# Kernel optimization log

Measured on AMD Instinct MI355X. Metric: run time of the kernel, lower is better.

Reference implementation:

```python
import jax, jax.numpy as jnp
import numpy as np

B, N = 32, 512
IN, HID, HEADS, OUT = 128, 32, 4, 128
NEG_SLOPE = 0.2


def _ln(x, g, b, eps=1e-5):
    mu = x.mean(-1, keepdims=True)
    var = ((x - mu) ** 2).mean(-1, keepdims=True)
    return (x - mu) * jax.lax.rsqrt(var + eps) * g + b


def _gat(x, adj_mask, W, a_src, a_dst, average):
    # x: [B,N,F], adj_mask: [B,1,N,N] bool, W: [F,H,D], a_*: [H,D]
    h = jnp.einsum('bnf,fhd->bnhd', x, W)                      # [B,N,H,D]
    e_src = jnp.einsum('bnhd,hd->bhn', h, a_src)               # [B,H,N]
    e_dst = jnp.einsum('bnhd,hd->bhn', h, a_dst)
    e = jax.nn.leaky_relu(e_src[:, :, :, None] + e_dst[:, :, None, :], NEG_SLOPE)  # [B,H,N,N]
    e = jnp.where(adj_mask, e, jnp.asarray(-1e9, e.dtype))
    att = jax.nn.softmax(e, axis=-1)                           # masked softmax over neighbors
    out = jnp.einsum('bhnm,bmhd->bnhd', att, h)                # aggregate neighbor features
    if average:
        return out.mean(axis=2)                                # [B,N,D]
    return out.reshape(out.shape[0], out.shape[1], -1)         # concat heads [B,N,H*D]


def setup_inputs() -> dict:
    key = jax.random.key(0)
    ks = jax.random.split(key, 16)
    def nrm(k, shape, scale=0.05):
        return jax.random.normal(k, shape, dtype=jnp.float32) * scale
    return {
        'x': jax.random.normal(ks[0], (B, N, IN), dtype=jnp.float32),
        'graph': jax.random.randint(ks[1], (B, N, N), 0, 2, dtype=jnp.int32),
        'W0': nrm(ks[2], (IN, HEADS, HID)),
        'a_src0': nrm(ks[3], (HEADS, HID)),
        'a_dst0': nrm(ks[4], (HEADS, HID)),
        'W1': nrm(ks[5], (HEADS * HID, 1, OUT)),
        'a_src1': nrm(ks[6], (1, OUT)),
        'a_dst1': nrm(ks[7], (1, OUT)),
        'ln1_g': jnp.ones((IN + OUT,), jnp.float32), 'ln1_b': jnp.zeros((IN + OUT,), jnp.float32),
        'lin_W': nrm(ks[8], (IN + OUT, OUT)), 'lin_b': jnp.zeros((OUT,), jnp.float32),
        'me_W0': nrm(ks[9], (OUT, OUT)), 'me_b0': jnp.zeros((OUT,), jnp.float32),
        'me_W1': nrm(ks[10], (OUT, OUT)), 'me_b1': jnp.zeros((OUT,), jnp.float32),
        'ln2_g': jnp.ones((OUT,), jnp.float32), 'ln2_b': jnp.zeros((OUT,), jnp.float32),
        'oh_W': nrm(ks[11], (OUT, OUT)), 'oh_b': jnp.zeros((OUT,), jnp.float32),
        'ln3_g': jnp.ones((OUT,), jnp.float32), 'ln3_b': jnp.zeros((OUT,), jnp.float32),
    }


def reference(x, graph, W0, a_src0, a_dst0, W1, a_src1, a_dst1,
              ln1_g, ln1_b, lin_W, lin_b, me_W0, me_b0, me_W1, me_b1,
              ln2_g, ln2_b, oh_W, oh_b, ln3_g, ln3_b):
    eye = jnp.eye(N, dtype=bool)
    adj_mask = ((graph > 0) | eye)[:, None, :, :]              # self-loops, [B,1,N,N]
    m = _gat(x, adj_mask, W0, a_src0, a_dst0, average=False)   # [B,N,HEADS*HID]
    m = jax.nn.elu(m)
    m = _gat(m, adj_mask, W1, a_src1, a_dst1, average=True)    # [B,N,OUT]
    m = _ln(jnp.concatenate([x, m], axis=-1), ln1_g, ln1_b)    # ln1
    m = m @ lin_W + lin_b                                      # linear
    enc = jax.nn.gelu(m @ me_W0 + me_b0, approximate=False) @ me_W1 + me_b1
    out = _ln(m + enc, ln2_g, ln2_b)                           # ln2(residual)
    out = jax.nn.gelu(out @ oh_W + oh_b, approximate=False)
    out = _ln(out, ln3_g, ln3_b)                               # LN inside output_head
    return out
```

## Files before the change

kernel.cpp:

```cpp
#include <hip/hip_runtime.h>
#include <cmath>


typedef unsigned short ushort_t;
typedef __attribute__((ext_vector_type(8))) short short8;
typedef __attribute__((ext_vector_type(4))) float f32x4;

__device__ __forceinline__ float gelu_f(float v) {
    return 0.5f * v * (1.0f + erff(v * 0.70710678118654752f));
}
__device__ __forceinline__ ushort_t f2bf(float x) {
    union { float f; unsigned u; } v; v.f = x;
    return (ushort_t)((v.u + 0x7FFFu + ((v.u >> 16) & 1u)) >> 16);
}
__device__ __forceinline__ ushort_t f2bf_t(float x) {
    union { float f; unsigned u; } v; v.f = x;
    return (ushort_t)(v.u >> 16);
}

__global__ __launch_bounds__(256) void prep_wt(const float* __restrict__ lin_W,
        const float* __restrict__ me_W0, const float* __restrict__ me_W1,
        const float* __restrict__ oh_W, const float* __restrict__ W0,
        const float* __restrict__ W1, ushort_t* __restrict__ WT) {
    int i = blockIdx.x * 256 + threadIdx.x;
    if (i < 32768)       { int c = i >> 8, k = i & 255;                   WT[i] = f2bf(lin_W[k * 128 + c]); }
    else if (i < 49152)  { int j = i - 32768;  int c = j >> 7, k = j & 127; WT[i] = f2bf(me_W0[k * 128 + c]); }
    else if (i < 65536)  { int j = i - 49152;  int c = j >> 7, k = j & 127; WT[i] = f2bf(me_W1[k * 128 + c]); }
    else if (i < 81920)  { int j = i - 65536;  int c = j >> 7, k = j & 127; WT[i] = f2bf(oh_W[k * 128 + c]); }
    else if (i < 98304)  { int j = i - 81920;  int c = j >> 7, k = j & 127; WT[i] = f2bf(W0[k * 128 + c]); }
    else if (i < 114688) { int j = i - 98304;  int c = j >> 7, k = j & 127; WT[i] = f2bf(W1[k * 128 + c]); }
}

__global__ __launch_bounds__(256) void pack_graph(const int* __restrict__ g,
                                                  unsigned* __restrict__ gm) {
    int idx = blockIdx.x * 256 + threadIdx.x;
    const int4* gp = (const int4*)g + (size_t)idx * 8;
    unsigned m = 0;
#pragma unroll
    for (int q = 0; q < 8; q++) {
        int4 v = gp[q];
        m |= (unsigned)(v.x > 0) << (q * 4 + 0);
        m |= (unsigned)(v.y > 0) << (q * 4 + 1);
        m |= (unsigned)(v.z > 0) << (q * 4 + 2);
        m |= (unsigned)(v.w > 0) << (q * 4 + 3);
    }
    gm[idx] = m;
}

__global__ __launch_bounds__(256) void gemm_mfma0(const float* __restrict__ X,
        const ushort_t* __restrict__ WTr, ushort_t* __restrict__ Ht,
        const float* __restrict__ a_s, const float* __restrict__ a_d,
        float* __restrict__ es, float* __restrict__ ed) {
    __shared__ __align__(16) ushort_t abuf[16 * 128];
    __shared__ __align__(16) ushort_t tb[128 * 24];
    __shared__ float2 ered[8 * 16];
    const int tid = threadIdx.x;
    const int row0 = blockIdx.x * 16;
    const int b = row0 >> 9, m0 = row0 & 511;
    const int w = tid >> 6, lane = tid & 63;
    const int quad = lane >> 4, lid = lane & 15;
    {
        int r = tid >> 4, g = tid & 15;
        const float4* src = (const float4*)(X + (row0 + r) * 128 + g * 8);
        float4 a = src[0], bb = src[1];
        short8 p;
        p[0] = (short)f2bf(a.x);  p[1] = (short)f2bf(a.y);
        p[2] = (short)f2bf(a.z);  p[3] = (short)f2bf(a.w);
        p[4] = (short)f2bf(bb.x); p[5] = (short)f2bf(bb.y);
        p[6] = (short)f2bf(bb.z); p[7] = (short)f2bf(bb.w);
        *(short8*)&abuf[r * 128 + ((g ^ (r & 7)) * 8)] = p;
    }
    __syncthreads();
    short8 af[4];
#pragma unroll
    for (int kc = 0; kc < 4; kc++)
        af[kc] = *(const short8*)&abuf[lid * 128 + (((kc * 4 + quad) ^ (lid & 7)) * 8)];
    f32x4 C[2];
#pragma unroll
    for (int i = 0; i < 2; i++) {
        int ct = w + 4 * i;
        const ushort_t* bp = WTr + (ct * 16 + lid) * 128 + quad * 8;
        C[i] = (f32x4){0.f, 0.f, 0.f, 0.f};
#pragma unroll
        for (int kc = 0; kc < 4; kc++) {
            short8 bf = *(const short8*)&bp[kc * 32];
            C[i] = __builtin_amdgcn_mfma_f32_16x16x32_bf16(af[kc], bf, C[i], 0, 0, 0);
        }
    }
#pragma unroll
    for (int i = 0; i < 2; i++) {
        int ct = w + 4 * i, col = ct * 16 + lid;
        float as_c = a_s[col], ad_c = a_d[col];
        float s0[4], d0[4];
#pragma unroll
        for (int r = 0; r < 4; r++) { s0[r] = C[i][r] * as_c; d0[r] = C[i][r] * ad_c; }
#pragma unroll
        for (int st = 1; st <= 8; st <<= 1)
#pragma unroll
            for (int r = 0; r < 4; r++) {
                s0[r] += __shfl_xor(s0[r], st);
                d0[r] += __shfl_xor(d0[r], st);
            }
        if (lid == 0) {
#pragma unroll
            for (int r = 0; r < 4; r++)
                ered[ct * 16 + quad * 4 + r] = make_float2(s0[r], d0[r]);
        }
#pragma unroll
        for (int r = 0; r < 4; r++)
            tb[col * 24 + quad * 4 + r] = f2bf(C[i][r]);
    }
    __syncthreads();
    if (tid < 64) {
        int row = tid & 15, h = tid >> 4;
        float2 pa = ered[(2 * h) * 16 + row], pb = ered[(2 * h + 1) * 16 + row];
        es[(b * 4 + h) * 512 + m0 + row] = pa.x + pb.x;
        ed[(b * 4 + h) * 512 + m0 + row] = pa.y + pb.y;
    }
    {
        int c = tid >> 1, half = tid & 1;
        *(short8*)&Ht[b * 65536 + c * 512 + m0 + half * 8] = *(const short8*)&tb[c * 24 + half * 8];
    }
}

__global__ __launch_bounds__(256) void gat0_gemm(const ushort_t* __restrict__ Ht0,
        const float* __restrict__ es0, const float* __restrict__ ed0,
        const unsigned* __restrict__ gmask, const ushort_t* __restrict__ W1T,
        const float* __restrict__ a_s, const float* __restrict__ a_d,
        ushort_t* __restrict__ Ht1, float* __restrict__ es1, float* __restrict__ ed1) {
    __shared__ __align__(16) char smem[33024];
    ushort_t* hsb  = (ushort_t*)smem;
    ushort_t* ps   = (ushort_t*)(smem + 16384);
    float*    eds  = (float*)(smem + 24576);
    float*    ess  = (float*)(smem + 32768);
    ushort_t* abuf = (ushort_t*)(smem + 16384);
    ushort_t* tb   = (ushort_t*)(smem + 24576);
    float2*   ered = (float2*)(smem + 30720);
    const int tid = threadIdx.x;
    const int b = blockIdx.y, n0 = blockIdx.x * 16;
    const int wv = tid >> 6, lane = tid & 63;
    const int quad = lane >> 4, lid = lane & 15;
    const int pn = tid >> 4, pg = (tid >> 1) & 7, ph = tid & 1;
    for (int i = tid; i < 2048; i += 256) eds[i] = ed0[b * 2048 + i];
    if (tid < 64) ess[tid] = es0[b * 2048 + (tid >> 4) * 512 + n0 + (tid & 15)];
    const unsigned* gmrow = gmask + (b * 512 + n0 + pn) * 16;
    const short8 onesf = {0x3F80, 0x3F80, 0x3F80, 0x3F80, 0x3F80, 0x3F80, 0x3F80, 0x3F80};
    f32x4 acc[2], dsf;
    acc[0] = (f32x4){0.f, 0.f, 0.f, 0.f};
    acc[1] = (f32x4){0.f, 0.f, 0.f, 0.f};
    dsf = (f32x4){0.f, 0.f, 0.f, 0.f};
    for (int mc = 0; mc < 512; mc += 64) {
        __syncthreads();
        {
            const ushort_t* src = Ht0 + b * 65536 + mc;
            for (int u = tid; u < 1024; u += 256) {
                int c = u >> 3, g = u & 7;
                *(short8*)&hsb[c * 64 + ((g ^ (c & 7)) * 8)] = *(const short8*)&src[c * 512 + g * 8];
            }
        }
        {
            int ng = n0 + pn, mbase = mc + pg * 8;
            unsigned mw = gmrow[mbase >> 5];
            unsigned mbits = (mw >> (mbase & 31)) & 0xffu;
            if ((unsigned)(ng - mbase) < 8u) mbits |= 1u << (ng - mbase);
#pragma unroll
            for (int hi = 0; hi < 2; hi++) {
                int hh = ph * 2 + hi;
                float es_v = ess[hh * 16 + pn];
                float4 e0v = *(const float4*)&eds[hh * 512 + mbase];
                float4 e1v = *(const float4*)&eds[hh * 512 + mbase + 4];
                float ev[8] = {e0v.x, e0v.y, e0v.z, e0v.w, e1v.x, e1v.y, e1v.z, e1v.w};
                short8 pk;
#pragma unroll
                for (int j = 0; j < 8; j++) {
                    float e = es_v + ev[j];
                    e = fmaxf(e, 0.2f * e);
                    e = ((mbits >> j) & 1u) ? e : -1e30f;
                    pk[j] = (short)f2bf_t(__expf(e));
                }
                int prow = hh * 16 + pn;
                *(short8*)&ps[prow * 64 + ((pg ^ (prow & 7)) * 8)] = pk;
            }
        }
        __syncthreads();
#pragma unroll
        for (int kc = 0; kc < 2; kc++) {
            const int gsw = ((kc * 4 + quad) ^ (lid & 7)) * 8;
            short8 a = *(const short8*)&ps[(wv * 16 + lid) * 64 + gsw];
            short8 b0 = *(const short8*)&hsb[(wv * 32 + lid) * 64 + gsw];
            short8 b1 = *(const short8*)&hsb[(wv * 32 + 16 + lid) * 64 + gsw];
            acc[0] = __builtin_amdgcn_mfma_f32_16x16x32_bf16(a, b0, acc[0], 0, 0, 0);
            acc[1] = __builtin_amdgcn_mfma_f32_16x16x32_bf16(a, b1, acc[1], 0, 0, 0);
            dsf = __builtin_amdgcn_mfma_f32_16x16x32_bf16(a, onesf, dsf, 0, 0, 0);
        }
    }
    __syncthreads();
#pragma unroll
    for (int reg = 0; reg < 4; reg++) {
        float inv = 1.0f / dsf[reg];
        int rw = quad * 4 + reg;
#pragma unroll
        for (int ch = 0; ch < 2; ch++) {
            float v = acc[ch][reg] * inv;
            v = v > 0.f ? v : expm1f(v);
            int col = wv * 32 + ch * 16 + lid;
            abuf[rw * 128 + (((col >> 3) ^ (rw & 7)) * 8) + (col & 7)] = f2bf(v);
        }
    }
    __syncthreads();
    short8 af[4];
#pragma unroll
    for (int kc = 0; kc < 4; kc++)
        af[kc] = *(const short8*)&abuf[lid * 128 + (((kc * 4 + quad) ^ (lid & 7)) * 8)];
    f32x4 C[2];
#pragma unroll
    for (int i = 0; i < 2; i++) {
        int ct = wv + 4 * i;
        const ushort_t* bp = W1T + (ct * 16 + lid) * 128 + quad * 8;
        C[i] = (f32x4){0.f, 0.f, 0.f, 0.f};
#pragma unroll
        for (int kc = 0; kc < 4; kc++) {
            short8 bf = *(const short8*)&bp[kc * 32];
            C[i] = __builtin_amdgcn_mfma_f32_16x16x32_bf16(af[kc], bf, C[i], 0, 0, 0);
        }
    }
#pragma unroll
    for (int i = 0; i < 2; i++) {
        int ct = wv + 4 * i, col = ct * 16 + lid;
        float as_c = a_s[col], ad_c = a_d[col];
        float s0[4], d0[4];
#pragma unroll
        for (int r = 0; r < 4; r++) { s0[r] = C[i][r] * as_c; d0[r] = C[i][r] * ad_c; }
#pragma unroll
        for (int st = 1; st <= 8; st <<= 1)
#pragma unroll
            for (int r = 0; r < 4; r++) {
                s0[r] += __shfl_xor(s0[r], st);
                d0[r] += __shfl_xor(d0[r], st);
            }
        if (lid == 0) {
#pragma unroll
            for (int r = 0; r < 4; r++)
                ered[ct * 16 + quad * 4 + r] = make_float2(s0[r], d0[r]);
        }
#pragma unroll
        for (int r = 0; r < 4; r++)
            tb[col * 24 + quad * 4 + r] = f2bf(C[i][r]);
    }
    __syncthreads();
    if (tid < 16) {
        float S = 0.f, D = 0.f;
#pragma unroll
        for (int ct = 0; ct < 8; ct++) { float2 p = ered[ct * 16 + tid]; S += p.x; D += p.y; }
        es1[b * 512 + n0 + tid] = S;
        ed1[b * 512 + n0 + tid] = D;
    }
    {
        int c = tid >> 1, half = tid & 1;
        *(short8*)&Ht1[b * 65536 + c * 512 + n0 + half * 8] = *(const short8*)&tb[c * 24 + half * 8];
    }
}

__global__ __launch_bounds__(256) void gat1_head(const ushort_t* __restrict__ Ht,
        const float* __restrict__ es1, const float* __restrict__ ed1,
        const unsigned* __restrict__ gmask, const float* __restrict__ x,
        const float* __restrict__ g1, const float* __restrict__ b1,
        const ushort_t* __restrict__ linT, const float* __restrict__ LB,
        const ushort_t* __restrict__ meT0, const float* __restrict__ B0,
        const ushort_t* __restrict__ meT1, const float* __restrict__ B1,
        const float* __restrict__ g2, const float* __restrict__ b2,
        const ushort_t* __restrict__ ohT, const float* __restrict__ ob,
        const float* __restrict__ g3, const float* __restrict__ b3,
        float* __restrict__ out) {
    __shared__ __align__(16) char smem[25472];
    ushort_t* hsb  = (ushort_t*)smem;
    ushort_t* ps   = (ushort_t*)(smem + 16384);
    float*    eds  = (float*)(smem + 18432);
    float*    ess  = (float*)(smem + 20480);
    ushort_t* ybuf = (ushort_t*)smem;
    ushort_t* abuf = (ushort_t*)(smem + 8192);
    ushort_t* tbuf = (ushort_t*)(smem + 12288);
    float*    gbuf = (float*)(smem + 16384);
    float2*   red  = (float2*)(smem + 24832);
    float2*   mvs  = (float2*)(smem + 25344);
    const int tid = threadIdx.x;
    const int b = blockIdx.y, n0 = blockIdx.x * 16;
    const int wv = tid >> 6, lane = tid & 63;
    const int quad = lane >> 4, lid = lane & 15;
    for (int i = tid; i < 512; i += 256) eds[i] = ed1[b * 512 + i];
    if (tid < 16) ess[tid] = es1[b * 512 + n0 + tid];
    const unsigned* gmrow = gmask + (b * 512 + n0 + (tid >> 3)) * 16;
    const short8 onesf = {0x3F80, 0x3F80, 0x3F80, 0x3F80, 0x3F80, 0x3F80, 0x3F80, 0x3F80};
    f32x4 acc[2], dsf;
    acc[0] = (f32x4){0.f, 0.f, 0.f, 0.f};
    acc[1] = (f32x4){0.f, 0.f, 0.f, 0.f};
    dsf = (f32x4){0.f, 0.f, 0.f, 0.f};
    for (int mc = 0; mc < 512; mc += 64) {
        __syncthreads();
        {
            const ushort_t* src = Ht + b * 65536 + mc;
            for (int u = tid; u < 1024; u += 256) {
                int c = u >> 3, g = u & 7;
                *(short8*)&hsb[c * 64 + ((g ^ (c & 7)) * 8)] = *(const short8*)&src[c * 512 + g * 8];
            }
        }
        if (tid < 128) {
            int pn = tid >> 3, pg = tid & 7;
            int ng = n0 + pn, mbase = mc + pg * 8;
            unsigned mw = gmrow[mbase >> 5];
            unsigned mbits = (mw >> (mbase & 31)) & 0xffu;
            if ((unsigned)(ng - mbase) < 8u) mbits |= 1u << (ng - mbase);
            float4 e0v = *(const float4*)&eds[mbase & 511];
            float4 e1v = *(const float4*)&eds[(mbase & 511) + 4];
            float ev[8] = {e0v.x, e0v.y, e0v.z, e0v.w, e1v.x, e1v.y, e1v.z, e1v.w};
            float es_v = ess[pn];
            short8 pk;
#pragma unroll
            for (int j = 0; j < 8; j++) {
                float e = es_v + ev[j];
                e = fmaxf(e, 0.2f * e);
                e = ((mbits >> j) & 1u) ? e : -1e30f;
                pk[j] = (short)f2bf_t(__expf(e));
            }
            *(short8*)&ps[pn * 64 + ((pg ^ (pn & 7)) * 8)] = pk;
        }
        __syncthreads();
#pragma unroll
        for (int kc = 0; kc < 2; kc++) {
            const int gsw = ((kc * 4 + quad) ^ (lid & 7)) * 8;
            short8 a = *(const short8*)&ps[lid * 64 + gsw];
            short8 b0 = *(const short8*)&hsb[(wv * 32 + lid) * 64 + gsw];
            short8 b1 = *(const short8*)&hsb[(wv * 32 + 16 + lid) * 64 + gsw];
            acc[0] = __builtin_amdgcn_mfma_f32_16x16x32_bf16(a, b0, acc[0], 0, 0, 0);
            acc[1] = __builtin_amdgcn_mfma_f32_16x16x32_bf16(a, b1, acc[1], 0, 0, 0);
            dsf = __builtin_amdgcn_mfma_f32_16x16x32_bf16(a, onesf, dsf, 0, 0, 0);
        }
    }
    __syncthreads();
#pragma unroll
    for (int reg = 0; reg < 4; reg++) {
        float inv = 1.0f / dsf[reg];
        int rw = quad * 4 + reg;
#pragma unroll
        for (int ch = 0; ch < 2; ch++)
            gbuf[rw * 132 + wv * 32 + ch * 16 + lid] = acc[ch][reg] * inv;
    }
    __syncthreads();
    const int r = tid >> 4, c16 = tid & 15;
    const float4* xp = (const float4*)(x + (b * 512 + n0 + r) * 128);
    float4 vv4[4];
    float s = 0.f, ss = 0.f;
#pragma unroll
    for (int i = 0; i < 4; i++) {
        int c4 = c16 * 4 + i;
        float4 v = (c4 < 32) ? xp[c4] : *(const float4*)&gbuf[r * 132 + (c4 - 32) * 4];
        vv4[i] = v;
        s += v.x + v.y + v.z + v.w;
        ss += v.x * v.x + v.y * v.y + v.z * v.z + v.w * v.w;
    }
#pragma unroll
    for (int st = 1; st <= 8; st <<= 1) { s += __shfl_xor(s, st); ss += __shfl_xor(ss, st); }
    if (c16 == 0) {
        float mu = s * (1.f / 256.f);
        float var = ss * (1.f / 256.f) - mu * mu;
        mvs[r] = make_float2(mu, rsqrtf(var + 1e-5f));
    }
    __syncthreads();
    {
        float mu = mvs[r].x, rstd = mvs[r].y;
#pragma unroll
        for (int half = 0; half < 2; half++) {
            int g = c16 * 2 + half, c0 = g * 8;
            float va[8] = {vv4[half * 2].x, vv4[half * 2].y, vv4[half * 2].z, vv4[half * 2].w,
                           vv4[half * 2 + 1].x, vv4[half * 2 + 1].y, vv4[half * 2 + 1].z, vv4[half * 2 + 1].w};
            short8 p;
#pragma unroll
            for (int e = 0; e < 8; e++)
                p[e] = (short)f2bf((va[e] - mu) * rstd * g1[c0 + e] + b1[c0 + e]);
            *(short8*)&ybuf[r * 256 + ((g ^ (r & 7)) * 8)] = p;
        }
    }
    __syncthreads();
    short8 af8[8];
#pragma unroll
    for (int ks = 0; ks < 8; ks++)
        af8[ks] = *(const short8*)&ybuf[lid * 256 + (((ks * 4 + quad) ^ (lid & 7)) * 8)];
    f32x4 M2[2];
#pragma unroll
    for (int i = 0; i < 2; i++) {
        int ct = wv + 4 * i;
        const ushort_t* bp = linT + (ct * 16 + lid) * 256 + quad * 8;
        M2[i] = (f32x4){0.f, 0.f, 0.f, 0.f};
#pragma unroll
        for (int ks = 0; ks < 8; ks++) {
            short8 bf = *(const short8*)&bp[ks * 32];
            M2[i] = __builtin_amdgcn_mfma_f32_16x16x32_bf16(af8[ks], bf, M2[i], 0, 0, 0);
        }
        float bias = LB[ct * 16 + lid];
#pragma unroll
        for (int reg = 0; reg < 4; reg++) M2[i][reg] += bias;
        int col = ct * 16 + lid, g = col >> 3, pos = col & 7;
#pragma unroll
        for (int reg = 0; reg < 4; reg++) {
            int rw = quad * 4 + reg;
            abuf[rw * 128 + ((g ^ (rw & 7)) * 8) + pos] = f2bf(M2[i][reg]);
        }
    }
    __syncthreads();
    short8 at[4];
#pragma unroll
    for (int kc = 0; kc < 4; kc++)
        at[kc] = *(const short8*)&abuf[lid * 128 + (((kc * 4 + quad) ^ (lid & 7)) * 8)];
#pragma unroll
    for (int i = 0; i < 2; i++) {
        int ct = wv + 4 * i;
        const ushort_t* bp = meT0 + (ct * 16 + lid) * 128 + quad * 8;
        f32x4 C = (f32x4){0.f, 0.f, 0.f, 0.f};
#pragma unroll
        for (int kc = 0; kc < 4; kc++) {
            short8 bf = *(const short8*)&bp[kc * 32];
            C = __builtin_amdgcn_mfma_f32_16x16x32_bf16(at[kc], bf, C, 0, 0, 0);
        }
        int col = ct * 16 + lid, g = col >> 3, pos = col & 7;
        float bias = B0[col];
#pragma unroll
        for (int reg = 0; reg < 4; reg++) {
            int rw = quad * 4 + reg;
            tbuf[rw * 128 + ((g ^ (rw & 7)) * 8) + pos] = f2bf(gelu_f(C[reg] + bias));
        }
    }
    __syncthreads();
#pragma unroll
    for (int kc = 0; kc < 4; kc++)
        at[kc] = *(const short8*)&tbuf[lid * 128 + (((kc * 4 + quad) ^ (lid & 7)) * 8)];
    f32x4 R[2];
    float sr[4] = {0.f, 0.f, 0.f, 0.f}, ssr[4] = {0.f, 0.f, 0.f, 0.f};
#pragma unroll
    for (int i = 0; i < 2; i++) {
        int ct = wv + 4 * i;
        const ushort_t* bp = meT1 + (ct * 16 + lid) * 128 + quad * 8;
        f32x4 C = (f32x4){0.f, 0.f, 0.f, 0.f};
#pragma unroll
        for (int kc = 0; kc < 4; kc++) {
            short8 bf = *(const short8*)&bp[kc * 32];
            C = __builtin_amdgcn_mfma_f32_16x16x32_bf16(at[kc], bf, C, 0, 0, 0);
        }
        float bias = B1[ct * 16 + lid];
#pragma unroll
        for (int reg = 0; reg < 4; reg++) {
            float v = M2[i][reg] + C[reg] + bias;
            R[i][reg] = v;
            sr[reg] += v; ssr[reg] += v * v;
        }
    }
#pragma unroll
    for (int st = 1; st <= 8; st <<= 1)
#pragma unroll
        for (int reg = 0; reg < 4; reg++) {
            sr[reg] += __shfl_xor(sr[reg], st);
            ssr[reg] += __shfl_xor(ssr[reg], st);
        }
    if (lid == 0) {
#pragma unroll
        for (int reg = 0; reg < 4; reg++)
            red[wv * 16 + quad * 4 + reg] = make_float2(sr[reg], ssr[reg]);
    }
    __syncthreads();
    float mu2[4], rstd2[4];
#pragma unroll
    for (int reg = 0; reg < 4; reg++) {
        float S = 0.f, SS = 0.f;
#pragma unroll
        for (int w4 = 0; w4 < 4; w4++) {
            float2 p = red[w4 * 16 + quad * 4 + reg];
            S += p.x; SS += p.y;
        }
        mu2[reg] = S * (1.f / 128.f);
        float var = SS * (1.f / 128.f) - mu2[reg] * mu2[reg];
        rstd2[reg] = rsqrtf(var + 1e-5f);
    }
#pragma unroll
    for (int i = 0; i < 2; i++) {
        int col = (wv + 4 * i) * 16 + lid, g = col >> 3, pos = col & 7;
        float gv = g2[col], bv = b2[col];
#pragma unroll
        for (int reg = 0; reg < 4; reg++) {
            int rw = quad * 4 + reg;
            float v = (R[i][reg] - mu2[reg]) * rstd2[reg] * gv + bv;
            tbuf[rw * 128 + ((g ^ (rw & 7)) * 8) + pos] = f2bf(v);
        }
    }
    __syncthreads();
#pragma unroll
    for (int kc = 0; kc < 4; kc++)
        at[kc] = *(const short8*)&tbuf[lid * 128 + (((kc * 4 + quad) ^ (lid & 7)) * 8)];
    f32x4 V[2];
#pragma unroll
    for (int reg = 0; reg < 4; reg++) { sr[reg] = 0.f; ssr[reg] = 0.f; }
#pragma unroll
    for (int i = 0; i < 2; i++) {
        int ct = wv + 4 * i;
        const ushort_t* bp = ohT + (ct * 16 + lid) * 128 + quad * 8;
        f32x4 C = (f32x4){0.f, 0.f, 0.f, 0.f};
#pragma unroll
        for (int kc = 0; kc < 4; kc++) {
            short8 bf = *(const short8*)&bp[kc * 32];
            C = __builtin_amdgcn_mfma_f32_16x16x32_bf16(at[kc], bf, C, 0, 0, 0);
        }
        float bias = ob[ct * 16 + lid];
#pragma unroll
        for (int reg = 0; reg < 4; reg++) {
            float v = gelu_f(C[reg] + bias);
            V[i][reg] = v;
            sr[reg] += v; ssr[reg] += v * v;
        }
    }
#pragma unroll
    for (int st = 1; st <= 8; st <<= 1)
#pragma unroll
        for (int reg = 0; reg < 4; reg++) {
            sr[reg] += __shfl_xor(sr[reg], st);
            ssr[reg] += __shfl_xor(ssr[reg], st);
        }
    if (lid == 0) {
#pragma unroll
        for (int reg = 0; reg < 4; reg++)
            red[wv * 16 + quad * 4 + reg] = make_float2(sr[reg], ssr[reg]);
    }
    __syncthreads();
#pragma unroll
    for (int reg = 0; reg < 4; reg++) {
        float S = 0.f, SS = 0.f;
#pragma unroll
        for (int w4 = 0; w4 < 4; w4++) {
            float2 p = red[w4 * 16 + quad * 4 + reg];
            S += p.x; SS += p.y;
        }
        mu2[reg] = S * (1.f / 128.f);
        float var = SS * (1.f / 128.f) - mu2[reg] * mu2[reg];
        rstd2[reg] = rsqrtf(var + 1e-5f);
    }
#pragma unroll
    for (int i = 0; i < 2; i++) {
        int col = (wv + 4 * i) * 16 + lid;
        float gv = g3[col], bv = b3[col];
#pragma unroll
        for (int reg = 0; reg < 4; reg++)
            out[(b * 512 + n0 + quad * 4 + reg) * 128 + col] =
                (V[i][reg] - mu2[reg]) * rstd2[reg] * gv + bv;
    }
}

extern "C" void kernel_launch(void* const* d_in, const int* in_sizes, int n_in,
                              void* d_out, int out_size, void* d_ws, size_t ws_size,
                              hipStream_t stream) {
    const float* x      = (const float*)d_in[0];
    const int*   graph  = (const int*)d_in[1];
    const float* a_src0 = (const float*)d_in[3];
    const float* a_dst0 = (const float*)d_in[4];
    const float* a_src1 = (const float*)d_in[6];
    const float* a_dst1 = (const float*)d_in[7];
    float* out = (float*)d_out;

    float* ws  = (float*)d_ws;
    ushort_t* Ht0  = (ushort_t*)ws;
    ushort_t* Ht1  = Ht0 + 2097152;
    float*    e0s  = ws + 2097152;
    float*    e0d  = e0s + 65536;
    float*    e1s  = e0d + 65536;
    float*    e1d  = e1s + 16384;
    ushort_t* WT   = (ushort_t*)(e1d + 16384);
    ushort_t* linT = WT;
    ushort_t* meT0 = WT + 32768;
    ushort_t* meT1 = WT + 49152;
    ushort_t* ohT  = WT + 65536;
    ushort_t* W0T  = WT + 81920;
    ushort_t* W1T  = WT + 98304;
    unsigned* gmask = (unsigned*)(WT + 114688);

    prep_wt<<<448, 256, 0, stream>>>((const float*)d_in[10], (const float*)d_in[12],
                                     (const float*)d_in[14], (const float*)d_in[18],
                                     (const float*)d_in[2], (const float*)d_in[5], WT);
    pack_graph<<<1024, 256, 0, stream>>>(graph, gmask);
    gemm_mfma0<<<1024, 256, 0, stream>>>(x, W0T, Ht0, a_src0, a_dst0, e0s, e0d);
    gat0_gemm<<<dim3(32, 32), 256, 0, stream>>>(Ht0, e0s, e0d, gmask, W1T,
                                                a_src1, a_dst1, Ht1, e1s, e1d);
    gat1_head<<<dim3(32, 32), 256, 0, stream>>>(Ht1, e1s, e1d, gmask, x,
                                                (const float*)d_in[8], (const float*)d_in[9],
                                                linT, (const float*)d_in[11],
                                                meT0, (const float*)d_in[13],
                                                meT1, (const float*)d_in[15],
                                                (const float*)d_in[16], (const float*)d_in[17],
                                                ohT, (const float*)d_in[19],
                                                (const float*)d_in[20], (const float*)d_in[21],
                                                out);
}
```

Baseline: 199.4 us.

## Double-buffer H tiles via direct global-to-LDS loads in GAT aggregation kernels

The two attention-aggregation kernels now stage each 64-column chunk of H directly from global memory into LDS using global_load_lds, double-buffered so the next chunk's load overlaps the current chunk's softmax-weight computation and MFMAs. To make the direct copy land in the bank-conflict-free layout, the producers write H already XOR-swizzled in global memory. Mask words and es values move into registers, and ed values are read from global or staged once rather than copied into LDS each iteration. LDS use grows, and correctness now depends on hand-placed vmcnt and lgkmcnt waits around raw barriers.

```diff
diff --git a/kernel.cpp b/kernel.cpp
--- a/kernel.cpp
+++ b/kernel.cpp
@@ -4,6 +4,7 @@
 
 typedef unsigned short ushort_t;
 typedef __attribute__((ext_vector_type(8))) short short8;
+typedef __attribute__((ext_vector_type(4))) short s16x4;
 typedef __attribute__((ext_vector_type(4))) float f32x4;
 
 __device__ __forceinline__ float gelu_f(float v) {
@@ -16,6 +17,20 @@
 __device__ __forceinline__ ushort_t f2bf_t(float x) {
     union { float f; unsigned u; } v; v.f = x;
     return (ushort_t)(v.u >> 16);
+}
+
+__device__ __forceinline__ void gload_lds16(const ushort_t* g, ushort_t* l) {
+    __builtin_amdgcn_global_load_lds((__attribute__((address_space(1))) void*)g,
+                                     (__attribute__((address_space(3))) void*)l, 16, 0, 0);
+}
+__device__ __forceinline__ void stage_chunk(const ushort_t* src, ushort_t* dst,
+                                            int wv, int lane) {
+#pragma unroll
+    for (int i = 0; i < 4; i++) {
+        int rbase = wv * 32 + i * 8;
+        gload_lds16(src + (rbase + (lane >> 3)) * 512 + (lane & 7) * 8,
+                    dst + rbase * 64);
+    }
 }
 
 __global__ __launch_bounds__(256) void prep_wt(const float* __restrict__ lin_W,
@@ -119,7 +134,9 @@
     }
     {
         int c = tid >> 1, half = tid & 1;
-        *(short8*)&Ht[b * 65536 + c * 512 + m0 + half * 8] = *(const short8*)&tb[c * 24 + half * 8];
+        int m = m0 + half * 8;
+        int msw = (m & ~63) | ((((m >> 3) ^ c) & 7) << 3);
+        *(short8*)&Ht[b * 65536 + c * 512 + msw] = *(const short8*)&tb[c * 24 + half * 8];
     }
 }
 
@@ -128,73 +145,90 @@
         const unsigned* __restrict__ gmask, const ushort_t* __restrict__ W1T,
         const float* __restrict__ a_s, const float* __restrict__ a_d,
         ushort_t* __restrict__ Ht1, float* __restrict__ es1, float* __restrict__ ed1) {
-    __shared__ __align__(16) char smem[33024];
-    ushort_t* hsb  = (ushort_t*)smem;
-    ushort_t* ps   = (ushort_t*)(smem + 16384);
-    float*    eds  = (float*)(smem + 24576);
-    float*    ess  = (float*)(smem + 32768);
-    ushort_t* abuf = (ushort_t*)(smem + 16384);
-    ushort_t* tb   = (ushort_t*)(smem + 24576);
-    float2*   ered = (float2*)(smem + 30720);
+    __shared__ __align__(16) char smem[40960];
+    ushort_t* hsb0 = (ushort_t*)smem;
+    ushort_t* hsb1 = (ushort_t*)(smem + 16384);
+    ushort_t* ps   = (ushort_t*)(smem + 32768);
+    ushort_t* abuf = (ushort_t*)(smem + 32768);
+    ushort_t* tb   = (ushort_t*)smem;
+    float2*   ered = (float2*)(smem + 6144);
     const int tid = threadIdx.x;
     const int b = blockIdx.y, n0 = blockIdx.x * 16;
     const int wv = tid >> 6, lane = tid & 63;
     const int quad = lane >> 4, lid = lane & 15;
     const int pn = tid >> 4, pg = (tid >> 1) & 7, ph = tid & 1;
-    for (int i = tid; i < 2048; i += 256) eds[i] = ed0[b * 2048 + i];
-    if (tid < 64) ess[tid] = es0[b * 2048 + (tid >> 4) * 512 + n0 + (tid & 15)];
-    const unsigned* gmrow = gmask + (b * 512 + n0 + pn) * 16;
+    const int ng = n0 + pn;
+    const ushort_t* hsrc = Ht0 + b * 65536;
+    const float es_r0 = es0[b * 2048 + (ph * 2) * 512 + ng];
+    const float es_r1 = es0[b * 2048 + (ph * 2 + 1) * 512 + ng];
+    const unsigned* gmrow = gmask + (b * 512 + ng) * 16;
+    unsigned mword[8];
+#pragma unroll
+    for (int t = 0; t < 8; t++) mword[t] = gmrow[2 * t + (pg >> 2)];
+    stage_chunk(hsrc, hsb0, wv, lane);
     const short8 onesf = {0x3F80, 0x3F80, 0x3F80, 0x3F80, 0x3F80, 0x3F80, 0x3F80, 0x3F80};
     f32x4 acc[2], dsf;
     acc[0] = (f32x4){0.f, 0.f, 0.f, 0.f};
     acc[1] = (f32x4){0.f, 0.f, 0.f, 0.f};
     dsf = (f32x4){0.f, 0.f, 0.f, 0.f};
-    for (int mc = 0; mc < 512; mc += 64) {
-        __syncthreads();
+#pragma unroll
+    for (int t = 0; t < 8; t++) {
+        const int mc = t * 64;
+        ushort_t* cbuf = (t & 1) ? hsb1 : hsb0;
+        const float* edg = ed0 + b * 2048 + mc + pg * 8;
+        float4 eA0 = *(const float4*)&edg[(ph * 2) * 512];
+        float4 eA1 = *(const float4*)&edg[(ph * 2) * 512 + 4];
+        float4 eB0 = *(const float4*)&edg[(ph * 2 + 1) * 512];
+        float4 eB1 = *(const float4*)&edg[(ph * 2 + 1) * 512 + 4];
+        if (t < 7) stage_chunk(hsrc + mc + 64, (t & 1) ? hsb0 : hsb1, wv, lane);
+        const int mbase = mc + pg * 8;
+        unsigned mb8 = (mword[t] >> ((pg & 3) * 8)) & 0xffu;
+        if ((unsigned)(ng - mbase) < 8u) mb8 |= 1u << (ng - mbase);
         {
-            const ushort_t* src = Ht0 + b * 65536 + mc;
-            for (int u = tid; u < 1024; u += 256) {
-                int c = u >> 3, g = u & 7;
-                *(short8*)&hsb[c * 64 + ((g ^ (c & 7)) * 8)] = *(const short8*)&src[c * 512 + g * 8];
+            float ev[8] = {eA0.x, eA0.y, eA0.z, eA0.w, eA1.x, eA1.y, eA1.z, eA1.w};
+            short8 pk;
+#pragma unroll
+            for (int j = 0; j < 8; j++) {
+                float e = es_r0 + ev[j];
+                e = fmaxf(e, 0.2f * e);
+                e = ((mb8 >> j) & 1u) ? e : -1e30f;
+                pk[j] = (short)f2bf_t(__expf(e));
             }
+            int prow = (ph * 2) * 16 + pn;
+            *(short8*)&ps[prow * 64 + ((pg ^ (prow & 7)) * 8)] = pk;
         }
         {
-            int ng = n0 + pn, mbase = mc + pg * 8;
-            unsigned mw = gmrow[mbase >> 5];
-            unsigned mbits = (mw >> (mbase & 31)) & 0xffu;
-            if ((unsigned)(ng - mbase) < 8u) mbits |= 1u << (ng - mbase);
-#pragma unroll
-            for (int hi = 0; hi < 2; hi++) {
-                int hh = ph * 2 + hi;
-                float es_v = ess[hh * 16 + pn];
-                float4 e0v = *(const float4*)&eds[hh * 512 + mbase];
-                float4 e1v = *(const float4*)&eds[hh * 512 + mbase + 4];
-                float ev[8] = {e0v.x, e0v.y, e0v.z, e0v.w, e1v.x, e1v.y, e1v.z, e1v.w};
-                short8 pk;
-#pragma unroll
-                for (int j = 0; j < 8; j++) {
-                    float e = es_v + ev[j];
-                    e = fmaxf(e, 0.2f * e);
-                    e = ((mbits >> j) & 1u) ? e : -1e30f;
-                    pk[j] = (short)f2bf_t(__expf(e));
-                }
-                int prow = hh * 16 + pn;
-                *(short8*)&ps[prow * 64 + ((pg ^ (prow & 7)) * 8)] = pk;
+            float ev[8] = {eB0.x, eB0.y, eB0.z, eB0.w, eB1.x, eB1.y, eB1.z, eB1.w};
+            short8 pk;
+#pragma unroll
+            for (int j = 0; j < 8; j++) {
+                float e = es_r1 + ev[j];
+                e = fmaxf(e, 0.2f * e);
+                e = ((mb8 >> j) & 1u) ? e : -1e30f;
+                pk[j] = (short)f2bf_t(__expf(e));
             }
-        }
-        __syncthreads();
+            int prow = (ph * 2 + 1) * 16 + pn;
+            *(short8*)&ps[prow * 64 + ((pg ^ (prow & 7)) * 8)] = pk;
+        }
+        if (t < 7) asm volatile("s_waitcnt vmcnt(4)" ::: "memory");
+        else       asm volatile("s_waitcnt vmcnt(0)" ::: "memory");
+        asm volatile("s_waitcnt lgkmcnt(0)" ::: "memory");
+        __builtin_amdgcn_s_barrier();
+        __builtin_amdgcn_sched_barrier(0);
 #pragma unroll
         for (int kc = 0; kc < 2; kc++) {
             const int gsw = ((kc * 4 + quad) ^ (lid & 7)) * 8;
             short8 a = *(const short8*)&ps[(wv * 16 + lid) * 64 + gsw];
-            short8 b0 = *(const short8*)&hsb[(wv * 32 + lid) * 64 + gsw];
-            short8 b1 = *(const short8*)&hsb[(wv * 32 + 16 + lid) * 64 + gsw];
+            short8 b0 = *(const short8*)&cbuf[(wv * 32 + lid) * 64 + gsw];
+            short8 b1 = *(const short8*)&cbuf[(wv * 32 + 16 + lid) * 64 + gsw];
             acc[0] = __builtin_amdgcn_mfma_f32_16x16x32_bf16(a, b0, acc[0], 0, 0, 0);
             acc[1] = __builtin_amdgcn_mfma_f32_16x16x32_bf16(a, b1, acc[1], 0, 0, 0);
             dsf = __builtin_amdgcn_mfma_f32_16x16x32_bf16(a, onesf, dsf, 0, 0, 0);
         }
-    }
-    __syncthreads();
+        __builtin_amdgcn_sched_barrier(0);
+        __builtin_amdgcn_s_barrier();
+        __builtin_amdgcn_sched_barrier(0);
+    }
 #pragma unroll
     for (int reg = 0; reg < 4; reg++) {
         float inv = 1.0f / dsf[reg];
@@ -257,7 +291,9 @@
     }
     {
         int c = tid >> 1, half = tid & 1;
-        *(short8*)&Ht1[b * 65536 + c * 512 + n0 + half * 8] = *(const short8*)&tb[c * 24 + half * 8];
+        int m = n0 + half * 8;
+        int msw = (m & ~63) | ((((m >> 3) ^ c) & 7) << 3);
+        *(short8*)&Ht1[b * 65536 + c * 512 + msw] = *(const short8*)&tb[c * 24 + half * 8];
     }
 }
 
@@ -272,11 +308,11 @@
         const ushort_t* __restrict__ ohT, const float* __restrict__ ob,
         const float* __restrict__ g3, const float* __restrict__ b3,
         float* __restrict__ out) {
-    __shared__ __align__(16) char smem[25472];
-    ushort_t* hsb  = (ushort_t*)smem;
-    ushort_t* ps   = (ushort_t*)(smem + 16384);
-    float*    eds  = (float*)(smem + 18432);
-    float*    ess  = (float*)(smem + 20480);
+    __shared__ __align__(16) char smem[36864];
+    ushort_t* hsb0 = (ushort_t*)smem;
+    ushort_t* hsb1 = (ushort_t*)(smem + 16384);
+    ushort_t* ps   = (ushort_t*)(smem + 32768);
+    float*    eds  = (float*)(smem + 34816);
     ushort_t* ybuf = (ushort_t*)smem;
     ushort_t* abuf = (ushort_t*)(smem + 8192);
     ushort_t* tbuf = (ushort_t*)(smem + 12288);
@@ -287,56 +323,63 @@
     const int b = blockIdx.y, n0 = blockIdx.x * 16;
     const int wv = tid >> 6, lane = tid & 63;
     const int quad = lane >> 4, lid = lane & 15;
-    for (int i = tid; i < 512; i += 256) eds[i] = ed1[b * 512 + i];
-    if (tid < 16) ess[tid] = es1[b * 512 + n0 + tid];
-    const unsigned* gmrow = gmask + (b * 512 + n0 + (tid >> 3)) * 16;
+    const int pn = tid >> 4, q = tid & 15, off = q * 4;
+    const int ng = n0 + pn;
+    const ushort_t* hsrc = Ht + b * 65536;
+    const float es_v = es1[b * 512 + ng];
+    const unsigned* gmrow = gmask + (b * 512 + ng) * 16;
+    unsigned mword[8];
+#pragma unroll
+    for (int t = 0; t < 8; t++) mword[t] = gmrow[2 * t + (q >> 3)];
+    float2 edv = ((const float2*)(ed1 + b * 512))[tid];
+    stage_chunk(hsrc, hsb0, wv, lane);
+    ((float2*)eds)[tid] = edv;
+    asm volatile("s_waitcnt lgkmcnt(0)" ::: "memory");
+    __builtin_amdgcn_s_barrier();
+    __builtin_amdgcn_sched_barrier(0);
     const short8 onesf = {0x3F80, 0x3F80, 0x3F80, 0x3F80, 0x3F80, 0x3F80, 0x3F80, 0x3F80};
     f32x4 acc[2], dsf;
     acc[0] = (f32x4){0.f, 0.f, 0.f, 0.f};
     acc[1] = (f32x4){0.f, 0.f, 0.f, 0.f};
     dsf = (f32x4){0.f, 0.f, 0.f, 0.f};
-    for (int mc = 0; mc < 512; mc += 64) {
-        __syncthreads();
-        {
-            const ushort_t* src = Ht + b * 65536 + mc;
-            for (int u = tid; u < 1024; u += 256) {
-                int c = u >> 3, g = u & 7;
-                *(short8*)&hsb[c * 64 + ((g ^ (c & 7)) * 8)] = *(const short8*)&src[c * 512 + g * 8];
-            }
-        }
-        if (tid < 128) {
-            int pn = tid >> 3, pg = tid & 7;
-            int ng = n0 + pn, mbase = mc + pg * 8;
-            unsigned mw = gmrow[mbase >> 5];
-            unsigned mbits = (mw >> (mbase & 31)) & 0xffu;
-            if ((unsigned)(ng - mbase) < 8u) mbits |= 1u << (ng - mbase);
-            float4 e0v = *(const float4*)&eds[mbase & 511];
-            float4 e1v = *(const float4*)&eds[(mbase & 511) + 4];
-            float ev[8] = {e0v.x, e0v.y, e0v.z, e0v.w, e1v.x, e1v.y, e1v.z, e1v.w};
-            float es_v = ess[pn];
-            short8 pk;
-#pragma unroll
-            for (int j = 0; j < 8; j++) {
-                float e = es_v + ev[j];
-                e = fmaxf(e, 0.2f * e);
-                e = ((mbits >> j) & 1u) ? e : -1e30f;
-                pk[j] = (short)f2bf_t(__expf(e));
-            }
-            *(short8*)&ps[pn * 64 + ((pg ^ (pn & 7)) * 8)] = pk;
-        }
-        __syncthreads();
+#pragma unroll
+    for (int t = 0; t < 8; t++) {
+        const int mc = t * 64;
+        ushort_t* cbuf = (t & 1) ? hsb1 : hsb0;
+        const int mbase = mc + off;
+        float4 ev4 = *(const float4*)&eds[mbase];
+        if (t < 7) stage_chunk(hsrc + mc + 64, (t & 1) ? hsb0 : hsb1, wv, lane);
+        unsigned mb4 = (mword[t] >> ((q & 7) * 4)) & 0xFu;
+        if ((unsigned)(ng - mbase) < 4u) mb4 |= 1u << (ng - mbase);
+        float ev[4] = {ev4.x, ev4.y, ev4.z, ev4.w};
+        s16x4 pk;
+#pragma unroll
+        for (int j = 0; j < 4; j++) {
+            float e = es_v + ev[j];
+            e = fmaxf(e, 0.2f * e);
+            e = ((mb4 >> j) & 1u) ? e : -1e30f;
+            pk[j] = (short)f2bf_t(__expf(e));
+        }
+        *(s16x4*)&ps[pn * 64 + (((off >> 3) ^ (pn & 7)) * 8) + (off & 7)] = pk;
+        if (t < 7) asm volatile("s_waitcnt vmcnt(4)" ::: "memory");
+        else       asm volatile("s_waitcnt vmcnt(0)" ::: "memory");
+        asm volatile("s_waitcnt lgkmcnt(0)" ::: "memory");
+        __builtin_amdgcn_s_barrier();
+        __builtin_amdgcn_sched_barrier(0);
 #pragma unroll
         for (int kc = 0; kc < 2; kc++) {
             const int gsw = ((kc * 4 + quad) ^ (lid & 7)) * 8;
             short8 a = *(const short8*)&ps[lid * 64 + gsw];
-            short8 b0 = *(const short8*)&hsb[(wv * 32 + lid) * 64 + gsw];
-            short8 b1 = *(const short8*)&hsb[(wv * 32 + 16 + lid) * 64 + gsw];
+            short8 b0 = *(const short8*)&cbuf[(wv * 32 + lid) * 64 + gsw];
+            short8 b1 = *(const short8*)&cbuf[(wv * 32 + 16 + lid) * 64 + gsw];
             acc[0] = __builtin_amdgcn_mfma_f32_16x16x32_bf16(a, b0, acc[0], 0, 0, 0);
             acc[1] = __builtin_amdgcn_mfma_f32_16x16x32_bf16(a, b1, acc[1], 0, 0, 0);
             dsf = __builtin_amdgcn_mfma_f32_16x16x32_bf16(a, onesf, dsf, 0, 0, 0);
         }
-    }
-    __syncthreads();
+        __builtin_amdgcn_sched_barrier(0);
+        __builtin_amdgcn_s_barrier();
+        __builtin_amdgcn_sched_barrier(0);
+    }
 #pragma unroll
     for (int reg = 0; reg < 4; reg++) {
         float inv = 1.0f / dsf[reg];
```

Result: faster. 185.9 us (-6.7%).
